# Kernel tuning notes

Hardware: AMD Instinct MI355X
Metric: run time of the kernel (lower is better)

## Reference

```python
import jax, jax.numpy as jnp
import numpy as np

B, T, M, VM = 64, 512, 8, 50  # batch, time, num_modules, rois per module
EPS = 1e-5  # BatchNorm eps


def setup_inputs() -> dict:
    key = jax.random.key(0)
    ks = jax.random.split(key, 12)
    x = jax.random.normal(ks[0], (B, M * VM, T, 1), jnp.float32)
    # learned adjacency, torch init = ones/V; perturb slightly
    PA = jnp.full((M, VM, VM), 1.0 / VM, jnp.float32) + 0.01 * jax.random.normal(ks[1], (M, VM, VM), jnp.float32)
    conv_w = jax.random.normal(ks[2], (M,), jnp.float32)          # 1x1 conv weight (1->1 chan) per module
    conv_b = 0.1 * jax.random.normal(ks[3], (M,), jnp.float32)
    bn_gamma = 1.0 + 0.1 * jax.random.normal(ks[4], (M,), jnp.float32)
    bn_beta = 0.1 * jax.random.normal(ks[5], (M,), jnp.float32)
    bn_mean = 0.1 * jax.random.normal(ks[6], (M,), jnp.float32)
    bn_var = jax.random.uniform(ks[7], (M,), jnp.float32) + 0.5   # positive
    w1 = jax.random.normal(ks[8], (M, 8), jnp.float32) * 0.5      # Linear(1,8) weight per module
    b1 = 0.1 * jax.random.normal(ks[9], (M, 8), jnp.float32)
    w2 = jax.random.normal(ks[10], (M, 8), jnp.float32) * 0.5     # Linear(8,1) weight per module
    b2 = 0.1 * jax.random.normal(ks[11], (M,), jnp.float32)
    return dict(x=x, PA=PA, conv_w=conv_w, conv_b=conv_b, bn_gamma=bn_gamma, bn_beta=bn_beta,
                bn_mean=bn_mean, bn_var=bn_var, w1=w1, b1=b1, w2=w2, b2=b2)


def reference(x, PA, conv_w, conv_b, bn_gamma, bn_beta, bn_mean, bn_var, w1, b1, w2, b2):
    # x: [B, V_total, T, 1]; torch permute(0,3,2,1) -> [B, C=1, T, V_total]
    xp = x[..., 0].transpose(0, 2, 1)                 # [B, T, V_total]
    xm = xp.reshape(B, T, M, VM)                      # contiguous module blocks == index_select
    # UnitGCN: x_agg = x @ A per module
    agg = jnp.einsum('btmv,mvw->btmw', xm, PA)        # [B, T, M, VM]
    # 1x1 conv (scalar per module) + BatchNorm2d(1) in eval mode + ReLU
    y = agg * conv_w[:, None] + conv_b[:, None]
    scale = bn_gamma / jnp.sqrt(bn_var + EPS)
    h = jax.nn.relu((y - bn_mean[:, None]) * scale[:, None] + bn_beta[:, None])
    # AttentionPooling: MLP(1->8->1) on channel dim, softmax over nodes, weighted sum
    hid = jnp.tanh(h[..., None] * w1[:, None, :] + b1[:, None, :])   # [B, T, M, VM, 8]
    score = jnp.einsum('btmvh,mh->btmv', hid, w2) + b2[:, None]      # [B, T, M, VM]
    attn = jax.nn.softmax(score, axis=3)
    pooled = jnp.sum(h * attn, axis=3)                # [B, T, M]
    # concat over modules on dim 1 -> [B, M, T, 1]
    return pooled.transpose(0, 2, 1)[..., None]
```

## Files before the change

### kernel.cpp

```cpp
#include <hip/hip_runtime.h>

#define BB 64
#define TT 512
#define MM 8
#define VMM 50
#define TBLK 128
#define EPSV 1e-5f

#define TN   1024
#define HMAX 16.0f
#define HSTEP (HMAX / TN)
#define INVH  (TN / HMAX)

#define WS_GT(m)   ((m) * TN)
#define WS_PAF(m)  (MM * TN + (m) * (8 * 64 * 4))
#define WS_NEED    ((MM * TN + MM * 8 * 64 * 4) * 4)

using short8  = __attribute__((ext_vector_type(8))) short;
using float4v = __attribute__((ext_vector_type(4))) float;

__device__ __forceinline__ float fast_rcp(float x) {
    return __builtin_amdgcn_rcpf(x);
}
__device__ __forceinline__ float fast_tanh(float x) {
    float e2 = __expf(2.0f * x);
    return fmaf(-2.0f, fast_rcp(e2 + 1.0f), 1.0f);
}
__device__ __forceinline__ unsigned f2bf(float f) {
    unsigned u = __float_as_uint(f);
    return (u + 0x7FFFu + ((u >> 16) & 1u)) >> 16;
}
__device__ __forceinline__ unsigned pack2(float lo, float hi) {
    return f2bf(lo) | (f2bf(hi) << 16);
}
__device__ __forceinline__ unsigned packh2(float lo, float hi) {
    unsigned short a = __builtin_bit_cast(unsigned short, (_Float16)lo);
    unsigned short b = __builtin_bit_cast(unsigned short, (_Float16)hi);
    return (unsigned)a | ((unsigned)b << 16);
}
__device__ __forceinline__ float h2f_lo(unsigned p) {
    return (float)__builtin_bit_cast(_Float16, (unsigned short)(p & 0xFFFFu));
}
__device__ __forceinline__ float h2f_hi(unsigned p) {
    return (float)__builtin_bit_cast(_Float16, (unsigned short)(p >> 16));
}

__global__ __launch_bounds__(256, 4)
void prep_kernel(const float* __restrict__ PA,
                 const float* __restrict__ w1,
                 const float* __restrict__ b1,
                 const float* __restrict__ w2,
                 const float* __restrict__ b2,
                 unsigned* __restrict__ ws)
{
    const int m = blockIdx.x;
    const int j = threadIdx.x;

    {
        float W1[8], B1[8], W2[8];
        float B2 = b2[m], sabs = 0.0f;
#pragma unroll
        for (int k = 0; k < 8; ++k) {
            W1[k] = w1[m * 8 + k];
            B1[k] = b1[m * 8 + k];
            W2[k] = w2[m * 8 + k];
            sabs += fabsf(W2[k]);
        }
        const float s0 = (B2 + sabs) - 8.0f;
        float gv[5];
#pragma unroll
        for (int k = 0; k < 5; ++k) {
            float h = (4 * j + k) * HSTEP;
            float s = B2 - s0;
#pragma unroll
            for (int i = 0; i < 8; ++i)
                s = fmaf(W2[i], fast_tanh(fmaf(h, W1[i], B1[i])), s);
            gv[k] = __expf(s);
        }
#pragma unroll
        for (int k = 0; k < 4; ++k)
            ws[WS_GT(m) + 4 * j + k] = packh2(gv[k], gv[k + 1] - gv[k]);
    }

    {
        const float* pa = PA + m * (VMM * VMM);
        uint4* dst = (uint4*)(ws + WS_PAF(m));
#pragma unroll
        for (int p = 0; p < 2; ++p) {
            int id   = j + p * 256;
            int wt   = id >> 7;
            int ks   = (id >> 6) & 1;
            int lane = id & 63;
            int w    = wt * 16 + (lane & 15);
            int vp0  = ks * 16 + (lane >> 4) * 4;
            unsigned u[4];
#pragma unroll
            for (int k = 0; k < 4; ++k) {
                int vp = vp0 + k, v0 = 2 * vp, v1 = v0 + 1;
                float a = (w < VMM && v0 < VMM) ? pa[v0 * VMM + w] : 0.0f;
                float c = (w < VMM && v1 < VMM) ? pa[v1 * VMM + w] : 0.0f;
                u[k] = pack2(a, c);
            }
            dst[(wt * 2 + ks) * 64 + lane] = make_uint4(u[0], u[1], u[2], u[3]);
        }
    }
}

__global__ __launch_bounds__(256, 4)
void intra_module_agg_kernel(const float* __restrict__ x,
                             const float* __restrict__ conv_w,
                             const float* __restrict__ conv_b,
                             const float* __restrict__ bn_gamma,
                             const float* __restrict__ bn_beta,
                             const float* __restrict__ bn_mean,
                             const float* __restrict__ bn_var,
                             const unsigned* __restrict__ ws,
                             float* __restrict__ out)
{
    const int blk = blockIdx.x;
    const int tq  = blk & 3;
    const int m   = (blk >> 2) & 7;
    const int b   = blk >> 5;
    const int j   = threadIdx.x;

    const int lane = j & 63, wv = j >> 6;
    const int q = lane >> 4, nl = lane & 15;

    __shared__ __align__(16) unsigned gt[TN];

    const float scale = bn_gamma[m] * __frsqrt_rn(bn_var[m] + EPSV);
    const float Amul  = conv_w[m] * scale;
    const float Cadd  = (conv_b[m] - bn_mean[m]) * scale + bn_beta[m];

    uint4 g = ((const uint4*)(ws + WS_GT(m)))[j];

    const uint4* paf = (const uint4*)(ws + WS_PAF(m));
    uint4 Araw[4][2];
#pragma unroll
    for (int wt = 0; wt < 4; ++wt)
#pragma unroll
        for (int ks = 0; ks < 2; ++ks)
            Araw[wt][ks] = paf[(wt * 2 + ks) * 64 + lane];

    const int t0 = tq * TBLK;
    float xr[2][16];
#pragma unroll
    for (int t2 = 0; t2 < 2; ++t2) {
        const int t = t0 + (wv * 2 + t2) * 16 + nl;
        const float* xg = x + ((b * (MM * VMM) + m * VMM) * TT + t);
#pragma unroll
        for (int jj = 0; jj < 8; ++jj) {
            xr[t2][jj] = xg[(q * 8 + jj) * TT];
        }
#pragma unroll
        for (int jj = 0; jj < 8; ++jj) {
            int v  = 32 + q * 8 + jj;
            int vc = (v < VMM) ? v : 0;
            float tv = xg[vc * TT];
            xr[t2][8 + jj] = (v < VMM) ? tv : 0.0f;
        }
    }

    *(uint4*)&gt[4 * j] = g;

    short8 Bf[2][2];
#pragma unroll
    for (int t2 = 0; t2 < 2; ++t2) {
#pragma unroll
        for (int ks = 0; ks < 2; ++ks) {
            uint4 u;
            u.x = pack2(xr[t2][8 * ks + 0], xr[t2][8 * ks + 1]);
            u.y = pack2(xr[t2][8 * ks + 2], xr[t2][8 * ks + 3]);
            u.z = pack2(xr[t2][8 * ks + 4], xr[t2][8 * ks + 5]);
            u.w = pack2(xr[t2][8 * ks + 6], xr[t2][8 * ks + 7]);
            Bf[t2][ks] = __builtin_bit_cast(short8, u);
        }
    }

    float4v C[2][4];
#pragma unroll
    for (int t2 = 0; t2 < 2; ++t2)
#pragma unroll
        for (int wt = 0; wt < 4; ++wt)
            C[t2][wt] = (float4v){0.f, 0.f, 0.f, 0.f};

#pragma unroll
    for (int t2 = 0; t2 < 2; ++t2) {
#pragma unroll
        for (int wt = 0; wt < 4; ++wt) {
            C[t2][wt] = __builtin_amdgcn_mfma_f32_16x16x32_bf16(
                __builtin_bit_cast(short8, Araw[wt][0]), Bf[t2][0], C[t2][wt], 0, 0, 0);
            C[t2][wt] = __builtin_amdgcn_mfma_f32_16x16x32_bf16(
                __builtin_bit_cast(short8, Araw[wt][1]), Bf[t2][1], C[t2][wt], 0, 0, 0);
        }
    }

    __syncthreads();

    const int obase = (b * MM + m) * TT + t0;
#pragma unroll
    for (int t2 = 0; t2 < 2; ++t2) {
        float se = 0.0f, sh = 0.0f;
#pragma unroll
        for (int wt = 0; wt < 4; ++wt) {
#pragma unroll
            for (int r = 0; r < 4; ++r) {
                const int w = wt * 16 + q * 4 + r;
                float h = fmaxf(fmaf(C[t2][wt][r], Amul, Cadd), 0.0f);
                float u = fminf(h, HMAX - 0.0005f) * INVH;
                int   i = (int)u;
                float fr = u - (float)i;
                unsigned p = gt[i];
                float e = (w < VMM) ? fmaf(fr, h2f_hi(p), h2f_lo(p)) : 0.0f;
                se += e;
                sh = fmaf(h, e, sh);
            }
        }
        se += __shfl_xor(se, 16, 64);
        se += __shfl_xor(se, 32, 64);
        sh += __shfl_xor(sh, 16, 64);
        sh += __shfl_xor(sh, 32, 64);
        if (q == 0)
            out[obase + (wv * 2 + t2) * 16 + nl] = sh * fast_rcp(se);
    }
}

#define RSTRIDE 36
__global__ __launch_bounds__(256, 4)
void mono_kernel(const float* __restrict__ x,
                 const float* __restrict__ PA,
                 const float* __restrict__ conv_w,
                 const float* __restrict__ conv_b,
                 const float* __restrict__ bn_gamma,
                 const float* __restrict__ bn_beta,
                 const float* __restrict__ bn_mean,
                 const float* __restrict__ bn_var,
                 const float* __restrict__ w1,
                 const float* __restrict__ b1,
                 const float* __restrict__ w2,
                 const float* __restrict__ b2,
                 float* __restrict__ out)
{
    const int blk = blockIdx.x;
    const int tq  = blk & 3;
    const int m   = (blk >> 2) & 7;
    const int b   = blk >> 5;
    const int j   = threadIdx.x;

    __shared__ __align__(16) unsigned xsu[TBLK * RSTRIDE];
    __shared__ __align__(16) unsigned psu[64 * RSTRIDE];
    __shared__ __align__(16) unsigned gt[TN];

    const float scale = bn_gamma[m] * __frsqrt_rn(bn_var[m] + EPSV);
    const float Amul  = conv_w[m] * scale;
    const float Cadd  = (conv_b[m] - bn_mean[m]) * scale + bn_beta[m];

    {
        const int t  = j >> 1;
        const int hf = j & 1;
        const float* xb = x + ((b * (MM * VMM) + m * VMM) * TT + tq * TBLK + t);
        unsigned* row = &xsu[t * RSTRIDE];
        const int vp0 = hf * 13;
#pragma unroll
        for (int i = 0; i < 13; ++i) {
            int vp = vp0 + i;
            float a = 0.0f, c = 0.0f;
            if (vp < 25) { a = xb[(2 * vp) * TT]; c = xb[(2 * vp + 1) * TT]; }
            row[vp] = pack2(a, c);
        }
        if (hf) {
#pragma unroll
            for (int vp = 26; vp < 32; ++vp) row[vp] = 0u;
        }
    }
    {
        const float* pa = PA + m * (VMM * VMM);
        const int w  = j & 63;
        const int vb = (j >> 6) * 8;
#pragma unroll
        for (int i = 0; i < 8; ++i) {
            int vp = vb + i, v0 = 2 * vp, v1 = v0 + 1;
            float a = (w < VMM && v0 < VMM) ? pa[v0 * VMM + w] : 0.0f;
            float c = (w < VMM && v1 < VMM) ? pa[v1 * VMM + w] : 0.0f;
            psu[w * RSTRIDE + vp] = pack2(a, c);
        }
    }
    {
        float W1[8], B1[8], W2[8];
        float B2 = b2[m], sabs = 0.0f;
#pragma unroll
        for (int k = 0; k < 8; ++k) {
            W1[k] = w1[m * 8 + k];
            B1[k] = b1[m * 8 + k];
            W2[k] = w2[m * 8 + k];
            sabs += fabsf(W2[k]);
        }
        const float s0 = (B2 + sabs) - 8.0f;
        float gv[5];
#pragma unroll
        for (int k = 0; k < 5; ++k) {
            float h = (4 * j + k) * HSTEP;
            float s = B2 - s0;
#pragma unroll
            for (int i = 0; i < 8; ++i)
                s = fmaf(W2[i], fast_tanh(fmaf(h, W1[i], B1[i])), s);
            gv[k] = __expf(s);
        }
#pragma unroll
        for (int k = 0; k < 4; ++k)
            gt[4 * j + k] = packh2(gv[k], gv[k + 1] - gv[k]);
    }

    __syncthreads();

    const int lane = j & 63, wv = j >> 6;
    const int q = lane >> 4, nl = lane & 15;

    short8 A[4][2];
#pragma unroll
    for (int wt = 0; wt < 4; ++wt)
#pragma unroll
        for (int ks = 0; ks < 2; ++ks)
            A[wt][ks] = *(const short8*)&psu[(wt * 16 + nl) * RSTRIDE + ks * 16 + q * 4];

    float4v C[2][4];
#pragma unroll
    for (int t2 = 0; t2 < 2; ++t2)
#pragma unroll
        for (int wt = 0; wt < 4; ++wt)
            C[t2][wt] = (float4v){0.f, 0.f, 0.f, 0.f};

#pragma unroll
    for (int t2 = 0; t2 < 2; ++t2) {
        const int trow = (wv * 2 + t2) * 16 + nl;
        short8 Bv0 = *(const short8*)&xsu[trow * RSTRIDE + 0 * 16 + q * 4];
        short8 Bv1 = *(const short8*)&xsu[trow * RSTRIDE + 1 * 16 + q * 4];
#pragma unroll
        for (int wt = 0; wt < 4; ++wt) {
            C[t2][wt] = __builtin_amdgcn_mfma_f32_16x16x32_bf16(A[wt][0], Bv0, C[t2][wt], 0, 0, 0);
            C[t2][wt] = __builtin_amdgcn_mfma_f32_16x16x32_bf16(A[wt][1], Bv1, C[t2][wt], 0, 0, 0);
        }
    }

    const int obase = (b * MM + m) * TT + tq * TBLK;
#pragma unroll
    for (int t2 = 0; t2 < 2; ++t2) {
        float se = 0.0f, sh = 0.0f;
#pragma unroll
        for (int wt = 0; wt < 4; ++wt) {
#pragma unroll
            for (int r = 0; r < 4; ++r) {
                const int w = wt * 16 + q * 4 + r;
                float h = fmaxf(fmaf(C[t2][wt][r], Amul, Cadd), 0.0f);
                float u = fminf(h, HMAX - 0.0005f) * INVH;
                int   i = (int)u;
                float fr = u - (float)i;
                unsigned p = gt[i];
                float e = (w < VMM) ? fmaf(fr, h2f_hi(p), h2f_lo(p)) : 0.0f;
                se += e;
                sh = fmaf(h, e, sh);
            }
        }
        se += __shfl_xor(se, 16, 64);
        se += __shfl_xor(se, 32, 64);
        sh += __shfl_xor(sh, 16, 64);
        sh += __shfl_xor(sh, 32, 64);
        if (q == 0)
            out[obase + (wv * 2 + t2) * 16 + nl] = sh * fast_rcp(se);
    }
}

extern "C" void kernel_launch(void* const* d_in, const int* in_sizes, int n_in,
                              void* d_out, int out_size, void* d_ws, size_t ws_size,
                              hipStream_t stream) {
    const float* x        = (const float*)d_in[0];
    const float* PA       = (const float*)d_in[1];
    const float* conv_w   = (const float*)d_in[2];
    const float* conv_b   = (const float*)d_in[3];
    const float* bn_gamma = (const float*)d_in[4];
    const float* bn_beta  = (const float*)d_in[5];
    const float* bn_mean  = (const float*)d_in[6];
    const float* bn_var   = (const float*)d_in[7];
    const float* w1       = (const float*)d_in[8];
    const float* b1       = (const float*)d_in[9];
    const float* w2       = (const float*)d_in[10];
    const float* b2       = (const float*)d_in[11];
    float* out = (float*)d_out;

    if (ws_size >= (size_t)WS_NEED) {
        unsigned* ws = (unsigned*)d_ws;
        prep_kernel<<<dim3(MM), dim3(256), 0, stream>>>(PA, w1, b1, w2, b2, ws);
        intra_module_agg_kernel<<<dim3(BB * MM * (TT / TBLK)), dim3(256), 0, stream>>>(
            x, conv_w, conv_b, bn_gamma, bn_beta, bn_mean, bn_var, ws, out);
    } else {
        mono_kernel<<<dim3(BB * MM * (TT / TBLK)), dim3(256), 0, stream>>>(
            x, PA, conv_w, conv_b, bn_gamma, bn_beta, bn_mean, bn_var,
            w1, b1, w2, b2, out);
    }
}
```

Before: 108.1 us.

## Process two time tiles per block with second tile's loads issued early

Each block now handles 256 time steps instead of 128, halving the grid. All x loads for the second half are issued before the first half's MFMA and epilogue, and an asm barrier keeps them in registers so their latency overlaps compute. The per-block setup (gate table into LDS, A fragments from the workspace, BN constants) is amortised over twice the work. The __syncthreads is replaced by a raw waitcnt plus s_barrier, and the occupancy hint is dropped from the launch bounds. This raises register pressure and halves block count (2048 → 1024), which may reduce latency hiding.

```diff
diff --git a/kernel.cpp b/kernel.cpp
--- a/kernel.cpp
+++ b/kernel.cpp
@@ -106,7 +106,7 @@
     }
 }
 
-__global__ __launch_bounds__(256, 4)
+__global__ __launch_bounds__(256)
 void intra_module_agg_kernel(const float* __restrict__ x,
                              const float* __restrict__ conv_w,
                              const float* __restrict__ conv_b,
@@ -118,9 +118,9 @@
                              float* __restrict__ out)
 {
     const int blk = blockIdx.x;
-    const int tq  = blk & 3;
-    const int m   = (blk >> 2) & 7;
-    const int b   = blk >> 5;
+    const int th  = blk & 1;
+    const int m   = (blk >> 1) & 7;
+    const int b   = blk >> 4;
     const int j   = threadIdx.x;
 
     const int lane = j & 63, wv = j >> 6;
@@ -132,96 +132,139 @@
     const float Amul  = conv_w[m] * scale;
     const float Cadd  = (conv_b[m] - bn_mean[m]) * scale + bn_beta[m];
 
-    uint4 g = ((const uint4*)(ws + WS_GT(m)))[j];
-
-    const uint4* paf = (const uint4*)(ws + WS_PAF(m));
-    uint4 Araw[4][2];
-#pragma unroll
-    for (int wt = 0; wt < 4; ++wt)
-#pragma unroll
-        for (int ks = 0; ks < 2; ++ks)
-            Araw[wt][ks] = paf[(wt * 2 + ks) * 64 + lane];
-
-    const int t0 = tq * TBLK;
-    float xr[2][16];
+    const int t0 = th * 256;
+    const float* xgb = x + ((b * (MM * VMM) + m * VMM) * TT);
+
+    float xa[2][16];
 #pragma unroll
     for (int t2 = 0; t2 < 2; ++t2) {
         const int t = t0 + (wv * 2 + t2) * 16 + nl;
-        const float* xg = x + ((b * (MM * VMM) + m * VMM) * TT + t);
-#pragma unroll
-        for (int jj = 0; jj < 8; ++jj) {
-            xr[t2][jj] = xg[(q * 8 + jj) * TT];
-        }
+        const float* xg = xgb + t;
+#pragma unroll
+        for (int jj = 0; jj < 8; ++jj)
+            xa[t2][jj] = xg[(q * 8 + jj) * TT];
 #pragma unroll
         for (int jj = 0; jj < 8; ++jj) {
             int v  = 32 + q * 8 + jj;
             int vc = (v < VMM) ? v : 0;
             float tv = xg[vc * TT];
-            xr[t2][8 + jj] = (v < VMM) ? tv : 0.0f;
-        }
-    }
+            xa[t2][8 + jj] = (v < VMM) ? tv : 0.0f;
+        }
+    }
+
+    uint4 g = ((const uint4*)(ws + WS_GT(m)))[j];
+    const uint4* paf = (const uint4*)(ws + WS_PAF(m));
+    uint4 Araw[4][2];
+#pragma unroll
+    for (int wt = 0; wt < 4; ++wt)
+#pragma unroll
+        for (int ks = 0; ks < 2; ++ks)
+            Araw[wt][ks] = paf[(wt * 2 + ks) * 64 + lane];
+
+    float xb_[2][16];
+#pragma unroll
+    for (int t2 = 0; t2 < 2; ++t2) {
+        const int t = t0 + TBLK + (wv * 2 + t2) * 16 + nl;
+        const float* xg = xgb + t;
+#pragma unroll
+        for (int jj = 0; jj < 8; ++jj)
+            xb_[t2][jj] = xg[(q * 8 + jj) * TT];
+#pragma unroll
+        for (int jj = 0; jj < 8; ++jj) {
+            int v  = 32 + q * 8 + jj;
+            int vc = (v < VMM) ? v : 0;
+            float tv = xg[vc * TT];
+            xb_[t2][8 + jj] = (v < VMM) ? tv : 0.0f;
+        }
+    }
+#pragma unroll
+    for (int t2 = 0; t2 < 2; ++t2)
+#pragma unroll
+        for (int i = 0; i < 16; ++i) asm volatile("" : "+v"(xb_[t2][i]));
 
     *(uint4*)&gt[4 * j] = g;
 
-    short8 Bf[2][2];
-#pragma unroll
-    for (int t2 = 0; t2 < 2; ++t2) {
+    short8 BfA[2][2];
+#pragma unroll
+    for (int t2 = 0; t2 < 2; ++t2)
 #pragma unroll
         for (int ks = 0; ks < 2; ++ks) {
             uint4 u;
-            u.x = pack2(xr[t2][8 * ks + 0], xr[t2][8 * ks + 1]);
-            u.y = pack2(xr[t2][8 * ks + 2], xr[t2][8 * ks + 3]);
-            u.z = pack2(xr[t2][8 * ks + 4], xr[t2][8 * ks + 5]);
-            u.w = pack2(xr[t2][8 * ks + 6], xr[t2][8 * ks + 7]);
-            Bf[t2][ks] = __builtin_bit_cast(short8, u);
-        }
-    }
-
-    float4v C[2][4];
-#pragma unroll
-    for (int t2 = 0; t2 < 2; ++t2)
-#pragma unroll
-        for (int wt = 0; wt < 4; ++wt)
-            C[t2][wt] = (float4v){0.f, 0.f, 0.f, 0.f};
-
-#pragma unroll
-    for (int t2 = 0; t2 < 2; ++t2) {
-#pragma unroll
-        for (int wt = 0; wt < 4; ++wt) {
-            C[t2][wt] = __builtin_amdgcn_mfma_f32_16x16x32_bf16(
-                __builtin_bit_cast(short8, Araw[wt][0]), Bf[t2][0], C[t2][wt], 0, 0, 0);
-            C[t2][wt] = __builtin_amdgcn_mfma_f32_16x16x32_bf16(
-                __builtin_bit_cast(short8, Araw[wt][1]), Bf[t2][1], C[t2][wt], 0, 0, 0);
-        }
-    }
-
-    __syncthreads();
+            u.x = pack2(xa[t2][8 * ks + 0], xa[t2][8 * ks + 1]);
+            u.y = pack2(xa[t2][8 * ks + 2], xa[t2][8 * ks + 3]);
+            u.z = pack2(xa[t2][8 * ks + 4], xa[t2][8 * ks + 5]);
+            u.w = pack2(xa[t2][8 * ks + 6], xa[t2][8 * ks + 7]);
+            BfA[t2][ks] = __builtin_bit_cast(short8, u);
+        }
+
+    asm volatile("s_waitcnt lgkmcnt(0)\n\ts_barrier" ::: "memory");
 
     const int obase = (b * MM + m) * TT + t0;
 #pragma unroll
-    for (int t2 = 0; t2 < 2; ++t2) {
-        float se = 0.0f, sh = 0.0f;
-#pragma unroll
-        for (int wt = 0; wt < 4; ++wt) {
-#pragma unroll
-            for (int r = 0; r < 4; ++r) {
-                const int w = wt * 16 + q * 4 + r;
-                float h = fmaxf(fmaf(C[t2][wt][r], Amul, Cadd), 0.0f);
-                float u = fminf(h, HMAX - 0.0005f) * INVH;
-                int   i = (int)u;
-                float fr = u - (float)i;
-                unsigned p = gt[i];
-                float e = (w < VMM) ? fmaf(fr, h2f_hi(p), h2f_lo(p)) : 0.0f;
-                se += e;
-                sh = fmaf(h, e, sh);
+    for (int half = 0; half < 2; ++half) {
+        short8 Bf[2][2];
+        if (half == 0) {
+#pragma unroll
+            for (int t2 = 0; t2 < 2; ++t2)
+#pragma unroll
+                for (int ks = 0; ks < 2; ++ks) Bf[t2][ks] = BfA[t2][ks];
+        } else {
+#pragma unroll
+            for (int t2 = 0; t2 < 2; ++t2)
+#pragma unroll
+                for (int ks = 0; ks < 2; ++ks) {
+                    uint4 u;
+                    u.x = pack2(xb_[t2][8 * ks + 0], xb_[t2][8 * ks + 1]);
+                    u.y = pack2(xb_[t2][8 * ks + 2], xb_[t2][8 * ks + 3]);
+                    u.z = pack2(xb_[t2][8 * ks + 4], xb_[t2][8 * ks + 5]);
+                    u.w = pack2(xb_[t2][8 * ks + 6], xb_[t2][8 * ks + 7]);
+                    Bf[t2][ks] = __builtin_bit_cast(short8, u);
+                }
+        }
+
+        float4v C[2][4];
+#pragma unroll
+        for (int t2 = 0; t2 < 2; ++t2)
+#pragma unroll
+            for (int wt = 0; wt < 4; ++wt)
+                C[t2][wt] = (float4v){0.f, 0.f, 0.f, 0.f};
+
+#pragma unroll
+        for (int t2 = 0; t2 < 2; ++t2)
+#pragma unroll
+            for (int wt = 0; wt < 4; ++wt) {
+                C[t2][wt] = __builtin_amdgcn_mfma_f32_16x16x32_bf16(
+                    __builtin_bit_cast(short8, Araw[wt][0]), Bf[t2][0], C[t2][wt], 0, 0, 0);
+                C[t2][wt] = __builtin_amdgcn_mfma_f32_16x16x32_bf16(
+                    __builtin_bit_cast(short8, Araw[wt][1]), Bf[t2][1], C[t2][wt], 0, 0, 0);
             }
-        }
-        se += __shfl_xor(se, 16, 64);
-        se += __shfl_xor(se, 32, 64);
-        sh += __shfl_xor(sh, 16, 64);
-        sh += __shfl_xor(sh, 32, 64);
-        if (q == 0)
-            out[obase + (wv * 2 + t2) * 16 + nl] = sh * fast_rcp(se);
+
+        const int ob = obase + half * TBLK;
+#pragma unroll
+        for (int t2 = 0; t2 < 2; ++t2) {
+            float se = 0.0f, sh = 0.0f;
+#pragma unroll
+            for (int wt = 0; wt < 4; ++wt) {
+#pragma unroll
+                for (int r = 0; r < 4; ++r) {
+                    const int w = wt * 16 + q * 4 + r;
+                    float h = fmaxf(fmaf(C[t2][wt][r], Amul, Cadd), 0.0f);
+                    float u = fminf(h, HMAX - 0.0005f) * INVH;
+                    int   i = (int)u;
+                    float fr = u - (float)i;
+                    unsigned p = gt[i];
+                    float e = (w < VMM) ? fmaf(fr, h2f_hi(p), h2f_lo(p)) : 0.0f;
+                    se += e;
+                    sh = fmaf(h, e, sh);
+                }
+            }
+            se += __shfl_xor(se, 16, 64);
+            se += __shfl_xor(se, 32, 64);
+            sh += __shfl_xor(sh, 16, 64);
+            sh += __shfl_xor(sh, 32, 64);
+            if (q == 0)
+                out[ob + (wv * 2 + t2) * 16 + nl] = sh * fast_rcp(se);
+        }
     }
 }
 
@@ -390,7 +433,7 @@
     if (ws_size >= (size_t)WS_NEED) {
         unsigned* ws = (unsigned*)d_ws;
         prep_kernel<<<dim3(MM), dim3(256), 0, stream>>>(PA, w1, b1, w2, b2, ws);
-        intra_module_agg_kernel<<<dim3(BB * MM * (TT / TBLK)), dim3(256), 0, stream>>>(
+        intra_module_agg_kernel<<<dim3(BB * MM * (TT / 256)), dim3(256), 0, stream>>>(
             x, conv_w, conv_b, bn_gamma, bn_beta, bn_mean, bn_var, ws, out);
     } else {
         mono_kernel<<<dim3(BB * MM * (TT / TBLK)), dim3(256), 0, stream>>>(
```

New measurement: 110.3 us. 2.1% more time.
